# Performance work log

Measured on AMD Instinct MI355X. Metric: run time of the kernel, lower is better.

Reference implementation:

```python
import jax, jax.numpy as jnp
import numpy as np

N_POOL = 500_000   # number of source neurons (value store size)
N_W = 1024         # number of unique (deduplicated) weight matrices
E = 1_000_000      # number of connections (neuron-input pairs)
D_IN = 16
D_OUT = 16


def setup_inputs() -> dict:
    key = jax.random.key(0)
    k1, k2, k3, k4 = jax.random.split(key, 4)
    values = jax.random.normal(k1, (N_POOL, D_IN), dtype=jnp.float32)
    weight = jax.random.normal(k2, (N_W, D_OUT, D_IN), dtype=jnp.float32)
    input_idx = jax.random.randint(k3, (E,), 0, N_POOL, dtype=jnp.int64) if jax.config.jax_enable_x64 else jax.random.randint(k3, (E,), 0, N_POOL).astype(jnp.int32)
    weight_idx = jax.random.randint(k4, (E,), 0, N_W).astype(jnp.int32)
    return {"values": values, "weight": weight, "input_idx": input_idx, "weight_idx": weight_idx}


def reference(values, weight, input_idx, weight_idx):
    # LINEAR_GATHER: gather input value vectors per connection  -> [E, D_IN]
    x = values[input_idx]
    # LINEAR_WEIGHTS_GATHER: gather weight matrices per connection -> [E, D_OUT, D_IN]
    w = weight[weight_idx]
    # LINEAR_LINEAR: per-connection matmul (w @ input_values) -> [E, D_OUT]
    y = jnp.einsum('eoi,ei->eo', w, x)
    return y
```

## Files before the change

### kernel.cpp

```cpp
#include <hip/hip_runtime.h>
#include <hip/hip_fp16.h>


#define D 16
#define WPB 4
#define TPB (WPB * 64)
#define MAXBLK 2048

__global__ __launch_bounds__(256) void linear_gather_mv(
    const float* __restrict__ values, const float* __restrict__ weight,
    const int* __restrict__ input_idx, const int* __restrict__ weight_idx,
    float* __restrict__ out, int E)
{
    int tid = blockIdx.x * blockDim.x + threadIdx.x;
    int e = tid >> 2;
    int j = tid & 3;
    if (e >= E) return;
    int ii = input_idx[e];
    int wi = weight_idx[e];
    const float4* xp = (const float4*)(values + (long long)ii * D);
    float4 x0 = xp[0], x1 = xp[1], x2 = xp[2], x3 = xp[3];
    const float4* wp = (const float4*)(weight + (long long)wi * (D * D) + j * (4 * D));
    float4 acc;
    float* accp = (float*)&acc;
    #pragma unroll
    for (int r = 0; r < 4; ++r) {
        float4 w0 = wp[r * 4 + 0], w1 = wp[r * 4 + 1], w2 = wp[r * 4 + 2], w3 = wp[r * 4 + 3];
        accp[r] = w0.x * x0.x + w0.y * x0.y + w0.z * x0.z + w0.w * x0.w
                + w1.x * x1.x + w1.y * x1.y + w1.z * x1.z + w1.w * x1.w
                + w2.x * x2.x + w2.y * x2.y + w2.z * x2.z + w2.w * x2.w
                + w3.x * x3.x + w3.y * x3.y + w3.z * x3.z + w3.w * x3.w;
    }
    ((float4*)out)[(long long)e * 4 + j] = acc;
}

__global__ __launch_bounds__(256) void wconv(
    const float* __restrict__ w, __half* __restrict__ wh, int n)
{
    int i = (blockIdx.x * 256 + threadIdx.x) * 4;
    if (i + 3 >= n) {
        for (int k = i; k < n; ++k) wh[k] = __float2half(w[k]);
        return;
    }
    float4 v = *(const float4*)(w + i);
    __half2 a = __floats2half2_rn(v.x, v.y);
    __half2 b = __floats2half2_rn(v.z, v.w);
    float2 packed;
    ((__half2*)&packed)[0] = a;
    ((__half2*)&packed)[1] = b;
    *(float2*)(wh + i) = packed;
}

__device__ __forceinline__ float2 wload(const __half* __restrict__ wh,
                                        int wi, int lane) {
    return ((const float2*)(wh + (long long)wi * (D * D)))[lane];
}

#define WLOAD8(C0, W0,W1,W2,W3,W4,W5,W6,W7) do {                               \
    W0 = wload(wh, __builtin_amdgcn_readlane(wcur, (C0)+0), lane);             \
    W1 = wload(wh, __builtin_amdgcn_readlane(wcur, (C0)+1), lane);             \
    W2 = wload(wh, __builtin_amdgcn_readlane(wcur, (C0)+2), lane);             \
    W3 = wload(wh, __builtin_amdgcn_readlane(wcur, (C0)+3), lane);             \
    W4 = wload(wh, __builtin_amdgcn_readlane(wcur, (C0)+4), lane);             \
    W5 = wload(wh, __builtin_amdgcn_readlane(wcur, (C0)+5), lane);             \
    W6 = wload(wh, __builtin_amdgcn_readlane(wcur, (C0)+6), lane);             \
    W7 = wload(wh, __builtin_amdgcn_readlane(wcur, (C0)+7), lane);             \
} while (0)

#define CONN1(C, WV) do {                                                      \
    const float4 xv = *(const float4*)(&xbuf[(C) * D + ((q ^ ((C) >> 4)) << 2)]); \
    float2 wlo = __half22float2(((const __half2*)&(WV))[0]);                   \
    float2 whi = __half22float2(((const __half2*)&(WV))[1]);                   \
    float p = wlo.x*xv.x + wlo.y*xv.y + whi.x*xv.z + whi.y*xv.w;               \
    p += __shfl_xor(p, 1);                                                     \
    p += __shfl_xor(p, 2);                                                     \
    if (q == 0 && (C) < nb) out[(long long)(k0 + (C)) * D + r] = p;            \
} while (0)

#define CONN8(C0, W0,W1,W2,W3,W4,W5,W6,W7) do {                                \
    CONN1((C0)+0, W0); CONN1((C0)+1, W1); CONN1((C0)+2, W2); CONN1((C0)+3, W3);\
    CONN1((C0)+4, W4); CONN1((C0)+5, W5); CONN1((C0)+6, W6); CONN1((C0)+7, W7);\
} while (0)

#define GATHER(BI) do {                                                        \
    int kl = (BI) * 64 + lane; if (kl >= E) kl = E - 1;                        \
    iv    = iidx[kl];                                                          \
    wnext = widx[kl];                                                          \
    int iiu;                                                                   \
    iiu = __shfl(iv,      g4); xq0 = ((const float4*)(values + (long long)iiu * D))[q]; \
    iiu = __shfl(iv, 16 + g4); xq1 = ((const float4*)(values + (long long)iiu * D))[q]; \
    iiu = __shfl(iv, 32 + g4); xq2 = ((const float4*)(values + (long long)iiu * D))[q]; \
    iiu = __shfl(iv, 48 + g4); xq3 = ((const float4*)(values + (long long)iiu * D))[q]; \
} while (0)

__global__ __launch_bounds__(TPB, 4) void direct_mv(
    const float* __restrict__ values, const __half* __restrict__ wh,
    const int* __restrict__ iidx, const int* __restrict__ widx,
    float* __restrict__ out, int E)
{
    __shared__ float xbuf_all[WPB * 64 * D];
    const int lane = threadIdx.x & 63;
    const int wid  = threadIdx.x >> 6;
    float* xbuf = xbuf_all + wid * (64 * D);
    const int g4 = lane >> 2;
    const int q  = lane & 3;
    const int r  = g4;

    const int nbatch = (E + 63) >> 6;
    const int gw = blockIdx.x * WPB + wid;
    const int GW = gridDim.x * WPB;
    if (gw >= nbatch) return;

    int iv, wnext;
    float4 xq0, xq1, xq2, xq3;
    GATHER(gw);

    for (int bi = gw; bi < nbatch; bi += GW) {
        ((float4*)&xbuf[( 0 + g4) * D])[q ^ 0] = xq0;
        ((float4*)&xbuf[(16 + g4) * D])[q ^ 1] = xq1;
        ((float4*)&xbuf[(32 + g4) * D])[q ^ 2] = xq2;
        ((float4*)&xbuf[(48 + g4) * D])[q ^ 3] = xq3;
        int wcur = wnext;
        int k0 = bi * 64;
        int nb = E - k0; if (nb > 64) nb = 64;

        int bn = bi + GW;
        if (bn < nbatch) GATHER(bn);

        float2 A0,A1,A2,A3,A4,A5,A6,A7;
        float2 B0,B1,B2,B3,B4,B5,B6,B7;
        WLOAD8( 0, A0,A1,A2,A3,A4,A5,A6,A7);
        WLOAD8( 8, B0,B1,B2,B3,B4,B5,B6,B7);
        CONN8 ( 0, A0,A1,A2,A3,A4,A5,A6,A7);
        WLOAD8(16, A0,A1,A2,A3,A4,A5,A6,A7);
        CONN8 ( 8, B0,B1,B2,B3,B4,B5,B6,B7);
        WLOAD8(24, B0,B1,B2,B3,B4,B5,B6,B7);
        CONN8 (16, A0,A1,A2,A3,A4,A5,A6,A7);
        WLOAD8(32, A0,A1,A2,A3,A4,A5,A6,A7);
        CONN8 (24, B0,B1,B2,B3,B4,B5,B6,B7);
        WLOAD8(40, B0,B1,B2,B3,B4,B5,B6,B7);
        CONN8 (32, A0,A1,A2,A3,A4,A5,A6,A7);
        WLOAD8(48, A0,A1,A2,A3,A4,A5,A6,A7);
        CONN8 (40, B0,B1,B2,B3,B4,B5,B6,B7);
        WLOAD8(56, B0,B1,B2,B3,B4,B5,B6,B7);
        CONN8 (48, A0,A1,A2,A3,A4,A5,A6,A7);
        CONN8 (56, B0,B1,B2,B3,B4,B5,B6,B7);
    }
}

extern "C" void kernel_launch(void* const* d_in, const int* in_sizes, int n_in,
                              void* d_out, int out_size, void* d_ws, size_t ws_size,
                              hipStream_t stream) {
    const float* values     = (const float*)d_in[0];
    const float* weight     = (const float*)d_in[1];
    const int*   input_idx  = (const int*)d_in[2];
    const int*   weight_idx = (const int*)d_in[3];
    float*       out        = (float*)d_out;

    int E = in_sizes[2];
    if (E <= 0) return;
    int NW = in_sizes[1] / (D * D);
    size_t need = (size_t)NW * D * D * sizeof(__half);

    if (ws_size < need) {
        int total_thr = E * 4;
        int grid = (total_thr + 255) / 256;
        hipLaunchKernelGGL(linear_gather_mv, dim3(grid), dim3(256), 0, stream,
                           values, weight, input_idx, weight_idx, out, E);
        return;
    }

    __half* wh = (__half*)d_ws;
    int nconv = NW * D * D;
    int cblk = (nconv / 4 + 255) / 256;
    hipLaunchKernelGGL(wconv, dim3(cblk), dim3(256), 0, stream,
                       weight, wh, nconv);

    int nbatch = (E + 63) >> 6;
    int nblk = (nbatch + WPB - 1) / WPB;
    if (nblk > MAXBLK) nblk = MAXBLK;
    hipLaunchKernelGGL(direct_mv, dim3(nblk), dim3(TPB), 0, stream,
                       values, wh, input_idx, weight_idx, out, E);
}
```

Measured before the change: 144.5 us.

## Process two connections per wavefront step with 16-byte weight loads and packed stores

Restructures the inner loop so each half-wave handles a different connection. Each lane loads a float4 (8 halves) of the weight matrix instead of a float2, which halves the number of load instructions and lets the dot-product reduction use one shuffle instead of two. Results are regathered by cross-lane shuffles so that each group of four lanes writes consecutive outputs, replacing the strided single-lane stores with more coalesced ones. The cost is extra shuffles, selects and more complex swizzled LDS addressing.

```diff
diff --git a/kernel.cpp b/kernel.cpp
--- a/kernel.cpp
+++ b/kernel.cpp
@@ -51,35 +51,40 @@
     *(float2*)(wh + i) = packed;
 }
 
-__device__ __forceinline__ float2 wload(const __half* __restrict__ wh,
-                                        int wi, int lane) {
-    return ((const float2*)(wh + (long long)wi * (D * D)))[lane];
-}
-
-#define WLOAD8(C0, W0,W1,W2,W3,W4,W5,W6,W7) do {                               \
-    W0 = wload(wh, __builtin_amdgcn_readlane(wcur, (C0)+0), lane);             \
-    W1 = wload(wh, __builtin_amdgcn_readlane(wcur, (C0)+1), lane);             \
-    W2 = wload(wh, __builtin_amdgcn_readlane(wcur, (C0)+2), lane);             \
-    W3 = wload(wh, __builtin_amdgcn_readlane(wcur, (C0)+3), lane);             \
-    W4 = wload(wh, __builtin_amdgcn_readlane(wcur, (C0)+4), lane);             \
-    W5 = wload(wh, __builtin_amdgcn_readlane(wcur, (C0)+5), lane);             \
-    W6 = wload(wh, __builtin_amdgcn_readlane(wcur, (C0)+6), lane);             \
-    W7 = wload(wh, __builtin_amdgcn_readlane(wcur, (C0)+7), lane);             \
+#define WPAIR(K, W0, W1) do {                                                  \
+    int a0 = __builtin_amdgcn_readlane(wcur, 4*(K)+0);                         \
+    int a1 = __builtin_amdgcn_readlane(wcur, 4*(K)+1);                         \
+    int a2 = __builtin_amdgcn_readlane(wcur, 4*(K)+2);                         \
+    int a3 = __builtin_amdgcn_readlane(wcur, 4*(K)+3);                         \
+    W0 = ((const float4*)(wh + (long long)(lh ? a1 : a0) * (D*D)))[hrow];      \
+    W1 = ((const float4*)(wh + (long long)(lh ? a3 : a2) * (D*D)))[hrow];      \
 } while (0)
 
-#define CONN1(C, WV) do {                                                      \
-    const float4 xv = *(const float4*)(&xbuf[(C) * D + ((q ^ ((C) >> 4)) << 2)]); \
-    float2 wlo = __half22float2(((const __half2*)&(WV))[0]);                   \
-    float2 whi = __half22float2(((const __half2*)&(WV))[1]);                   \
-    float p = wlo.x*xv.x + wlo.y*xv.y + whi.x*xv.z + whi.y*xv.w;               \
-    p += __shfl_xor(p, 1);                                                     \
-    p += __shfl_xor(p, 2);                                                     \
-    if (q == 0 && (C) < nb) out[(long long)(k0 + (C)) * D + r] = p;            \
+#define STEP(CC, WV, YS) do {                                                  \
+    int c  = (CC) + lh;                                                        \
+    int sw = c >> 4;                                                           \
+    int a0 = c * (D*4) + ((((h)<<1) ^ sw) << 4);                               \
+    const float4 xlo = *(const float4*)((const char*)xbuf + a0);               \
+    const float4 xhi = *(const float4*)((const char*)xbuf + (a0 ^ 16));        \
+    float2 f0 = __half22float2(((const __half2*)&(WV))[0]);                    \
+    float2 f1 = __half22float2(((const __half2*)&(WV))[1]);                    \
+    float2 f2 = __half22float2(((const __half2*)&(WV))[2]);                    \
+    float2 f3 = __half22float2(((const __half2*)&(WV))[3]);                    \
+    float p = f0.x*xlo.x + f0.y*xlo.y + f1.x*xlo.z + f1.y*xlo.w                \
+            + f2.x*xhi.x + f2.y*xhi.y + f3.x*xhi.z + f3.y*xhi.w;               \
+    p += __shfl_xor(p, 1);            \
+    YS = p;                                                                    \
 } while (0)
 
-#define CONN8(C0, W0,W1,W2,W3,W4,W5,W6,W7) do {                                \
-    CONN1((C0)+0, W0); CONN1((C0)+1, W1); CONN1((C0)+2, W2); CONN1((C0)+3, W3);\
-    CONN1((C0)+4, W4); CONN1((C0)+5, W5); CONN1((C0)+6, W6); CONN1((C0)+7, W7);\
+#define COMP4(K, W0, W1) do {                                                  \
+    float ys0, ys1;                                                            \
+    STEP(4*(K)+0, W0, ys0);                                                    \
+    STEP(4*(K)+2, W1, ys1);                                                    \
+    float v0 = __shfl(ys0, srcl);                                              \
+    float v1 = __shfl(ys1, srcl);                                              \
+    float yv = (lane & 2) ? v1 : v0;                                           \
+    int cc = 4*(K) + (lane & 3);                                               \
+    if (cc < nb) outb[(long long)cc * D + pr] = yv;                            \
 } while (0)
 
 #define GATHER(BI) do {                                                        \
@@ -104,7 +109,11 @@
     float* xbuf = xbuf_all + wid * (64 * D);
     const int g4 = lane >> 2;
     const int q  = lane & 3;
-    const int r  = g4;
+    const int lh   = lane >> 5;
+    const int h    = lane & 1;
+    const int hrow = lane & 31;
+    const int pr   = lane >> 2;
+    const int srcl = 32 * (lane & 1) + 2 * (lane >> 2);
 
     const int nbatch = (E + 63) >> 6;
     const int gw = blockIdx.x * WPB + wid;
@@ -123,28 +132,30 @@
         int wcur = wnext;
         int k0 = bi * 64;
         int nb = E - k0; if (nb > 64) nb = 64;
+        float* outb = out + (long long)k0 * D;
 
         int bn = bi + GW;
         if (bn < nbatch) GATHER(bn);
 
-        float2 A0,A1,A2,A3,A4,A5,A6,A7;
-        float2 B0,B1,B2,B3,B4,B5,B6,B7;
-        WLOAD8( 0, A0,A1,A2,A3,A4,A5,A6,A7);
-        WLOAD8( 8, B0,B1,B2,B3,B4,B5,B6,B7);
-        CONN8 ( 0, A0,A1,A2,A3,A4,A5,A6,A7);
-        WLOAD8(16, A0,A1,A2,A3,A4,A5,A6,A7);
-        CONN8 ( 8, B0,B1,B2,B3,B4,B5,B6,B7);
-        WLOAD8(24, B0,B1,B2,B3,B4,B5,B6,B7);
-        CONN8 (16, A0,A1,A2,A3,A4,A5,A6,A7);
-        WLOAD8(32, A0,A1,A2,A3,A4,A5,A6,A7);
-        CONN8 (24, B0,B1,B2,B3,B4,B5,B6,B7);
-        WLOAD8(40, B0,B1,B2,B3,B4,B5,B6,B7);
-        CONN8 (32, A0,A1,A2,A3,A4,A5,A6,A7);
-        WLOAD8(48, A0,A1,A2,A3,A4,A5,A6,A7);
-        CONN8 (40, B0,B1,B2,B3,B4,B5,B6,B7);
-        WLOAD8(56, B0,B1,B2,B3,B4,B5,B6,B7);
-        CONN8 (48, A0,A1,A2,A3,A4,A5,A6,A7);
-        CONN8 (56, B0,B1,B2,B3,B4,B5,B6,B7);
+        float4 P0, P1, Q0, Q1;
+        WPAIR( 0, P0, P1);
+        WPAIR( 1, Q0, Q1);
+        COMP4( 0, P0, P1); WPAIR( 2, P0, P1);
+        COMP4( 1, Q0, Q1); WPAIR( 3, Q0, Q1);
+        COMP4( 2, P0, P1); WPAIR( 4, P0, P1);
+        COMP4( 3, Q0, Q1); WPAIR( 5, Q0, Q1);
+        COMP4( 4, P0, P1); WPAIR( 6, P0, P1);
+        COMP4( 5, Q0, Q1); WPAIR( 7, Q0, Q1);
+        COMP4( 6, P0, P1); WPAIR( 8, P0, P1);
+        COMP4( 7, Q0, Q1); WPAIR( 9, Q0, Q1);
+        COMP4( 8, P0, P1); WPAIR(10, P0, P1);
+        COMP4( 9, Q0, Q1); WPAIR(11, Q0, Q1);
+        COMP4(10, P0, P1); WPAIR(12, P0, P1);
+        COMP4(11, Q0, Q1); WPAIR(13, Q0, Q1);
+        COMP4(12, P0, P1); WPAIR(14, P0, P1);
+        COMP4(13, Q0, Q1); WPAIR(15, Q0, Q1);
+        COMP4(14, P0, P1);
+        COMP4(15, Q0, Q1);
     }
 }
 
```

Result: faster. 131.9 us (-8.8%).
